# Kernel tuning notes

Measured on AMD Instinct MI355X. Metric: run time of the kernel, lower is better.

Reference implementation:

```python
import jax, jax.numpy as jnp
import numpy as np

P = 4; PSIZE = 16; EPS = 1e-8; LAM = 1e-3; MF = 2.0; ITERS = 2
BATCH = 64; A = 64; B = 8; C = 16; D = 16; E = 10


def _conv2d(x, w, b, stride, pad):
    y = jax.lax.conv_general_dilated(x, w, (stride, stride), [(pad, pad), (pad, pad)],
                                     dimension_numbers=('NCHW', 'OIHW', 'NCHW'))
    return y + b[None, :, None, None]


def _patches(x, K, stride):
    # x: (b, H, W, F) -> (b, oh, ow, K, K, F) sliding KxK windows with given stride
    b, H, W, F = x.shape
    oh = (H - K) // stride + 1
    ow = (W - K) // stride + 1
    ih = jnp.arange(oh) * stride
    iw = jnp.arange(ow) * stride
    p = x[:, ih[:, None] + jnp.arange(K)[None, :]]          # (b, oh, K, W, F)
    p = p[:, :, :, iw[:, None] + jnp.arange(K)[None, :]]    # (b, oh, K, ow, K, F)
    return p.transpose(0, 1, 3, 2, 4, 5), oh, ow


def _fuzzy_routing(v, a_in, beta_u, beta_a):
    # Fuzzy (c-means style) routing. v: (n, N, Cout, PSIZE) votes, a_in: (n, N).
    n, N, Cc, _ = v.shape
    r = jnp.full((n, N, Cc), 1.0 / Cc, dtype=v.dtype)
    aw = a_in[:, :, None]
    for t in range(ITERS):
        rm = (r ** MF) * aw                                             # fuzzified, activation-weighted
        coeff = rm / (jnp.sum(rm, axis=1, keepdims=True) + EPS)         # (n, N, C)
        mu = jnp.einsum('bnc,bncp->bcp', coeff, v)                      # (n, C, PSIZE)
        if t < ITERS - 1:
            dist = jnp.sum((v - mu[:, None]) ** 2, axis=-1) + EPS       # (n, N, C)
            inv = dist ** (-1.0 / (MF - 1.0))
            r = inv / (jnp.sum(inv, axis=2, keepdims=True) + EPS)
    sigma_sq = jnp.einsum('bnc,bncp->bcp', coeff, (v - mu[:, None]) ** 2) + EPS
    r_sum = jnp.sum((r ** MF) * aw, axis=1)                             # (n, C)
    cost = (beta_u[None, :, None] + 0.5 * jnp.log(sigma_sq)) * r_sum[:, :, None]
    a_out = jax.nn.sigmoid(LAM * (beta_a[None, :] - jnp.sum(cost, axis=2)))
    return mu, a_out


def _conv_caps(pose, a, W, beta_u, beta_a, K, stride):
    # pose: (b, H, W, Bi, PSIZE), a: (b, H, W, Bi); W: (K*K*Bi, Co, P, P)
    b, H, Wd, Bi, _ = pose.shape
    Co = W.shape[1]
    pp, oh, ow = _patches(pose.reshape(b, H, Wd, Bi * PSIZE), K, stride)
    ap, _, _ = _patches(a, K, stride)
    n = b * oh * ow
    pp = pp.reshape(n, K * K * Bi, P, P)
    ap = ap.reshape(n, K * K * Bi)
    v = jnp.einsum('nipq,icqr->nicpr', pp, W).reshape(n, K * K * Bi, Co, PSIZE)
    mu, a_out = _fuzzy_routing(v, ap, beta_u, beta_a)
    return mu.reshape(b, oh, ow, Co, PSIZE), a_out.reshape(b, oh, ow, Co)


def _class_caps(pose, a, W, beta_u, beta_a):
    # K=1, weight-shared over positions, with coordinate addition.
    b, H, Wd, Bi, _ = pose.shape
    Co = W.shape[1]
    v = jnp.einsum('bhwipq,icqr->bhwicpr', pose.reshape(b, H, Wd, Bi, P, P), W)
    v = v.reshape(b, H, Wd, Bi, Co, PSIZE)
    ch = (jnp.arange(H, dtype=v.dtype) / H)[None, :, None, None, None]
    cw = (jnp.arange(Wd, dtype=v.dtype) / Wd)[None, None, :, None, None]
    v = v.at[..., 0].add(ch)
    v = v.at[..., 1].add(cw)
    v = v.reshape(b, H * Wd * Bi, Co, PSIZE)
    return _fuzzy_routing(v, a.reshape(b, -1), beta_u, beta_a)


def setup_inputs():
    key = jax.random.key(0)
    ks = jax.random.split(key, 8)
    return {
        'x': jax.random.normal(ks[0], (BATCH, 1, 32, 32), jnp.float32),
        'conv1_w': jax.random.normal(ks[1], (A, 1, 5, 5), jnp.float32) * 0.1,
        'conv1_b': jnp.zeros((A,), jnp.float32),
        'bn_g': jnp.ones((A,), jnp.float32),
        'bn_b': jnp.zeros((A,), jnp.float32),
        'bn_mean': jnp.zeros((A,), jnp.float32),
        'bn_var': jnp.ones((A,), jnp.float32),
        'prim_pose_w': jax.random.normal(ks[2], (B * PSIZE, A, 1, 1), jnp.float32) * 0.1,
        'prim_pose_b': jnp.zeros((B * PSIZE,), jnp.float32),
        'prim_a_w': jax.random.normal(ks[3], (B, A, 1, 1), jnp.float32) * 0.1,
        'prim_a_b': jnp.zeros((B,), jnp.float32),
        'w1': jax.random.normal(ks[4], (3 * 3 * B, C, P, P), jnp.float32),
        'bu1': jnp.zeros((C,), jnp.float32),
        'ba1': jnp.zeros((C,), jnp.float32),
        'w2': jax.random.normal(ks[5], (3 * 3 * C, D, P, P), jnp.float32),
        'bu2': jnp.zeros((D,), jnp.float32),
        'ba2': jnp.zeros((D,), jnp.float32),
        'wc': jax.random.normal(ks[6], (D, E, P, P), jnp.float32),
        'buc': jnp.zeros((E,), jnp.float32),
        'bac': jnp.zeros((E,), jnp.float32),
    }


def reference(x, conv1_w, conv1_b, bn_g, bn_b, bn_mean, bn_var,
              prim_pose_w, prim_pose_b, prim_a_w, prim_a_b,
              w1, bu1, ba1, w2, bu2, ba2, wc, buc, bac):
    y = _conv2d(x, conv1_w, conv1_b, 2, 2)                               # (b, A, 16, 16)
    inv_std = jax.lax.rsqrt(bn_var + 1e-3)
    y = (y - bn_mean[None, :, None, None]) * (bn_g * inv_std)[None, :, None, None] + bn_b[None, :, None, None]
    y = jax.nn.relu(y)
    pose = _conv2d(y, prim_pose_w, prim_pose_b, 1, 0)                    # (b, B*16, 16, 16)
    a = jax.nn.sigmoid(_conv2d(y, prim_a_w, prim_a_b, 1, 0))             # (b, B, 16, 16)
    b_, _, H, Wd = a.shape
    pose = pose.transpose(0, 2, 3, 1).reshape(b_, H, Wd, B, PSIZE)
    a = a.transpose(0, 2, 3, 1)
    pose1, a1 = _conv_caps(pose, a, w1, bu1, ba1, 3, 2)
    pose2, a2 = _conv_caps(pose1, a1, w2, bu2, ba2, 3, 1)
    _, a_class = _class_caps(pose2, a2, wc, buc, bac)                    # (b, E)
    return a_class
```

## Files before the change

kernel.cpp:

```cpp
#include <hip/hip_runtime.h>
#include <math.h>

#define EPS_ 1e-8f
#define LAM_ 1e-3f

__global__ __launch_bounds__(256) void k_conv_transw(
    const float* __restrict__ x, const float* __restrict__ cw, const float* __restrict__ cb,
    const float* __restrict__ g, const float* __restrict__ bb,
    const float* __restrict__ mean, const float* __restrict__ var,
    float* __restrict__ y,
    const float* __restrict__ w1, const float* __restrict__ w2, const float* __restrict__ wc,
    const float* __restrict__ pw, const float* __restrict__ pb,
    const float* __restrict__ aw, const float* __restrict__ ab,
    float* __restrict__ w1t, float* __restrict__ w2t, float* __restrict__ wct,
    float* __restrict__ wpt)
{
    if (blockIdx.x < 4096) {
        int t = blockIdx.x * 256 + threadIdx.x;
        int ch = t & 63, w = (t >> 6) & 15, h = (t >> 10) & 15, b = t >> 14;
        const float* xb = x + b * 1024;
        const float* wc_ = cw + ch * 25;
        float acc = cb[ch];
        #pragma unroll
        for (int kh = 0; kh < 5; ++kh) {
            int ih = h * 2 - 2 + kh;
            if (ih < 0 || ih > 31) continue;
            #pragma unroll
            for (int kw = 0; kw < 5; ++kw) {
                int iw = w * 2 - 2 + kw;
                if (iw < 0 || iw > 31) continue;
                acc = fmaf(xb[ih * 32 + iw], wc_[kh * 5 + kw], acc);
            }
        }
        float v = (acc - mean[ch]) * (g[ch] * rsqrtf(var[ch] + 1e-3f)) + bb[ch];
        y[t] = fmaxf(v, 0.f);
    } else {
        int t = (blockIdx.x - 4096) * 256 + threadIdx.x;
        if (t < 3616 * 16) {
            int m = t >> 4, e = t & 15, r = e >> 2, q = e & 3;
            const float* src; float* dst;
            if (m < 1152)      { src = w1 + m * 16;          dst = w1t + m * 16; }
            else if (m < 3456) { src = w2 + (m - 1152) * 16; dst = w2t + (m - 1152) * 16; }
            else               { src = wc + (m - 3456) * 16; dst = wct + (m - 3456) * 16; }
            dst[e] = src[q * 4 + r];
        } else if (t < 3616 * 16 + 65 * 136) {
            int idx = t - 3616 * 16;
            int o = idx % 136, j = idx / 136;
            float v;
            if (j == 64)       v = (o < 128) ? pb[o] : ab[o - 128];
            else if (o < 128)  v = pw[o * 64 + j];
            else               v = aw[(o - 128) * 64 + j];
            wpt[j * 136 + o] = v;
        }
    }
}

__global__ __launch_bounds__(256) void k_prim(
    const float* __restrict__ y, const float* __restrict__ wpt,
    float* __restrict__ poseP, float* __restrict__ aP)
{
    int t = blockIdx.x * 256 + threadIdx.x;
    if (t >= 16384 * 34) return;
    int oq = t % 34;
    int pos = t / 34;
    const float* yp = y + pos * 64;
    float4 acc = *(const float4*)(wpt + 64 * 136 + oq * 4);
    #pragma unroll
    for (int j0 = 0; j0 < 64; j0 += 4) {
        float4 y4 = *(const float4*)(yp + j0);
        float4 w0 = *(const float4*)(wpt + (j0 + 0) * 136 + oq * 4);
        float4 w1 = *(const float4*)(wpt + (j0 + 1) * 136 + oq * 4);
        float4 w2 = *(const float4*)(wpt + (j0 + 2) * 136 + oq * 4);
        float4 w3 = *(const float4*)(wpt + (j0 + 3) * 136 + oq * 4);
        acc.x = fmaf(y4.x, w0.x, fmaf(y4.y, w1.x, fmaf(y4.z, w2.x, fmaf(y4.w, w3.x, acc.x))));
        acc.y = fmaf(y4.x, w0.y, fmaf(y4.y, w1.y, fmaf(y4.z, w2.y, fmaf(y4.w, w3.y, acc.y))));
        acc.z = fmaf(y4.x, w0.z, fmaf(y4.y, w1.z, fmaf(y4.z, w2.z, fmaf(y4.w, w3.z, acc.z))));
        acc.w = fmaf(y4.x, w0.w, fmaf(y4.y, w1.w, fmaf(y4.z, w2.w, fmaf(y4.w, w3.w, acc.w))));
    }
    if (oq < 32) {
        ((float4*)(poseP + pos * 128))[oq] = acc;
    } else {
        int oo = (oq - 32) * 4;
        float* ad = aP + pos * 8 + oo;
        ad[0] = 1.f / (1.f + __expf(-acc.x));
        ad[1] = 1.f / (1.f + __expf(-acc.y));
        ad[2] = 1.f / (1.f + __expf(-acc.z));
        ad[3] = 1.f / (1.f + __expf(-acc.w));
    }
}

template<int N, int C, int K, int S, int H, int W, int Bi, int OH, int OW>
__global__ __launch_bounds__(64) void k_caps_w1(
    const float* __restrict__ pose_in,
    const float* __restrict__ a_in,
    const float* __restrict__ Wt,
    const float* __restrict__ bu, const float* __restrict__ ba,
    float* __restrict__ pose_out,
    float* __restrict__ a_out)
{
    static_assert(C == 16 && N % 8 == 0, "");
    constexpr int NIT = N / 4;
    constexpr int NP  = NIT / 2;

    __shared__ __align__(16) float pp[N * 16];
    __shared__ float ap[N];

    const int lane = threadIdx.x;
    const int n_ = blockIdx.x;
    const int b = n_ / (OH * OW);
    const int rem = n_ % (OH * OW);
    const int oh = rem / OW, ow = rem % OW;

    for (int idx = lane; idx < N * 4; idx += 64) {
        int i = idx >> 2, f = idx & 3;
        int bi = i % Bi, k2 = i / Bi;
        int sw = ow * S + (k2 % K), sh = oh * S + (k2 / K);
        ((float4*)(pp + i * 16))[f] =
            ((const float4*)(pose_in + (((b * H + sh) * W + sw) * Bi + bi) * 16))[f];
    }
    for (int i = lane; i < N; i += 64) {
        int bi = i % Bi, k2 = i / Bi;
        int sw = ow * S + (k2 % K), sh = oh * S + (k2 / K);
        ap[i] = a_in[((b * H + sh) * W + sw) * Bi + bi];
    }
    __syncthreads();

    float suma = 0.f;
    for (int i = lane; i < N; i += 64) suma += ap[i];
    #pragma unroll
    for (int m = 1; m < 64; m <<= 1) suma += __shfl_xor(suma, m, 64);
    const float inv0 = __builtin_amdgcn_rcpf(suma + (float)(C * C) * EPS_);

    const int ig = (lane >> 4) & 3, cc = lane & 15;

    float mu[16];
    #pragma unroll
    for (int e2 = 0; e2 < 16; ++e2) mu[e2] = 0.f;
    for (int ii = 0; ii < NIT; ++ii) {
        int i = ig + ii * 4;
        const float4* pi4 = (const float4*)(pp + i * 16);
        const float4* wt4 = (const float4*)(Wt + (i * C + cc) * 16);
        float4 pv[4] = { pi4[0], pi4[1], pi4[2], pi4[3] };
        float4 wv[4] = { wt4[0], wt4[1], wt4[2], wt4[3] };
        float co = ap[i] * inv0;
        #pragma unroll
        for (int e2 = 0; e2 < 16; ++e2) {
            float4 p4 = pv[e2 >> 2], w4 = wv[e2 & 3];
            float v = p4.x * w4.x + p4.y * w4.y + p4.z * w4.z + p4.w * w4.w;
            mu[e2] = fmaf(co, v, mu[e2]);
        }
    }
    #pragma unroll
    for (int e2 = 0; e2 < 16; ++e2) {
        mu[e2] += __shfl_xor(mu[e2], 16, 64);
        mu[e2] += __shfl_xor(mu[e2], 32, 64);
    }

    float Sv[16], Sv2[16];
    #pragma unroll
    for (int e2 = 0; e2 < 16; ++e2) { Sv[e2] = 0.f; Sv2[e2] = 0.f; }
    float rsum = 0.f;
    for (int jj = 0; jj < NP; ++jj) {
        int i0 = ig + (2 * jj) * 4;
        int i1 = i0 + 4;
        const float4* p04 = (const float4*)(pp + i0 * 16);
        const float4* w04 = (const float4*)(Wt + (i0 * C + cc) * 16);
        const float4* p14 = (const float4*)(pp + i1 * 16);
        const float4* w14 = (const float4*)(Wt + (i1 * C + cc) * 16);
        float4 pv0[4] = { p04[0], p04[1], p04[2], p04[3] };
        float4 wv0[4] = { w04[0], w04[1], w04[2], w04[3] };
        float4 pv1[4] = { p14[0], p14[1], p14[2], p14[3] };
        float4 wv1[4] = { w14[0], w14[1], w14[2], w14[3] };
        float vv0[16], vv1[16];
        float d0 = EPS_, d1 = EPS_;
        #pragma unroll
        for (int e2 = 0; e2 < 16; ++e2) {
            float4 a4 = pv0[e2 >> 2], x4 = wv0[e2 & 3];
            float4 b4 = pv1[e2 >> 2], y4 = wv1[e2 & 3];
            float v0 = a4.x * x4.x + a4.y * x4.y + a4.z * x4.z + a4.w * x4.w;
            float v1 = b4.x * y4.x + b4.y * y4.y + b4.z * y4.z + b4.w * y4.w;
            vv0[e2] = v0; vv1[e2] = v1;
            float e0 = v0 - mu[e2];
            float e1 = v1 - mu[e2];
            d0 = fmaf(e0, e0, d0);
            d1 = fmaf(e1, e1, d1);
        }
        float inv_0 = __builtin_amdgcn_rcpf(d0);
        float inv_1 = __builtin_amdgcn_rcpf(d1);
        float s0 = inv_0, s1 = inv_1;
        #pragma unroll
        for (int m = 1; m < 16; m <<= 1) {
            s0 += __shfl_xor(s0, m, 64);
            s1 += __shfl_xor(s1, m, 64);
        }
        float r10 = inv_0 * __builtin_amdgcn_rcpf(s0 + EPS_);
        float r11 = inv_1 * __builtin_amdgcn_rcpf(s1 + EPS_);
        float rm0 = r10 * r10 * ap[i0];
        float rm1 = r11 * r11 * ap[i1];
        rsum += rm0 + rm1;
        #pragma unroll
        for (int e2 = 0; e2 < 16; ++e2) {
            float rv0 = rm0 * vv0[e2];
            float rv1 = rm1 * vv1[e2];
            Sv[e2] += rv0 + rv1;
            Sv2[e2] = fmaf(rv0, vv0[e2], fmaf(rv1, vv1[e2], Sv2[e2]));
        }
    }
    #pragma unroll
    for (int e2 = 0; e2 < 16; ++e2) {
        Sv[e2] += __shfl_xor(Sv[e2], 16, 64);
        Sv[e2] += __shfl_xor(Sv[e2], 32, 64);
        Sv2[e2] += __shfl_xor(Sv2[e2], 16, 64);
        Sv2[e2] += __shfl_xor(Sv2[e2], 32, 64);
    }
    rsum += __shfl_xor(rsum, 16, 64);
    rsum += __shfl_xor(rsum, 32, 64);

    const float id = 1.f / (rsum + EPS_);
    const float S0 = rsum * id;
    const float buc_ = bu[cc];
    float cs = 0.f;
    float4 outv[4];
    #pragma unroll
    for (int e2 = 0; e2 < 16; ++e2) {
        float sv = Sv[e2] * id;
        float sv2 = Sv2[e2] * id;
        float sigma = fmaxf(sv2 + sv * sv * (S0 - 2.f), 0.f) + EPS_;
        cs += (buc_ + 0.5f * __logf(sigma)) * rsum;
        ((float*)outv)[e2] = sv;
    }
    if (lane < 16) {
        float4* pd = (float4*)(pose_out + (n_ * C + cc) * 16);
        pd[0] = outv[0]; pd[1] = outv[1]; pd[2] = outv[2]; pd[3] = outv[3];
        a_out[n_ * C + cc] = 1.f / (1.f + __expf(-(LAM_ * (ba[cc] - cs))));
    }
}

template<int N, int C, int H, int W, int Bi, int BLK>
__global__ __launch_bounds__(BLK) void k_caps_class(
    const float* __restrict__ pose_in, const float* __restrict__ a_in,
    const float* __restrict__ Wt,
    const float* __restrict__ bu, const float* __restrict__ ba,
    float* __restrict__ a_out)
{
    constexpr int NW  = BLK / 64;
    constexpr int NIG = BLK / 16;
    constexpr int NIT = (N + NIG - 1) / NIG;

    __shared__ __align__(16) float pp[N * 16];
    __shared__ float ap[N];
    __shared__ float coeff0[N];
    __shared__ float mu0[16 * 17];
    __shared__ float red1[NW * C * 17];
    __shared__ float red2[NW * C * 17];
    __shared__ float redr[NW * C];

    const int t = threadIdx.x;
    const int lane = t & 63;
    const int w = t >> 6;
    const int b = blockIdx.x;

    for (int idx = t; idx < N * 4; idx += BLK) {
        int i = idx >> 2, f = idx & 3;
        int bi = i % Bi;
        int hw = i / Bi;
        int sw = hw % W, sh = hw / W;
        const float4* src = (const float4*)(pose_in + (((b * H + sh) * W + sw) * Bi + bi) * 16);
        ((float4*)(pp + i * 16))[f] = src[f];
    }
    for (int i = t; i < N; i += BLK) {
        int bi = i % Bi;
        int hw = i / Bi;
        int sw = hw % W, sh = hw / W;
        ap[i] = a_in[((b * H + sh) * W + sw) * Bi + bi];
    }
    __syncthreads();

    {
        float part = 0.f;
        for (int i = t; i < N; i += BLK) part += ap[i];
        #pragma unroll
        for (int m = 1; m < 64; m <<= 1) part += __shfl_xor(part, m, 64);
        if (lane == 0) red1[w] = part;
        __syncthreads();
        float s = 0.f;
        #pragma unroll
        for (int ww = 0; ww < NW; ++ww) s += red1[ww];
        float inv0 = __builtin_amdgcn_rcpf(s + (float)(C * C) * EPS_);
        for (int i = t; i < N; i += BLK) coeff0[i] = ap[i] * inv0;
        __syncthreads();
    }

    const int ig = t >> 4, cc = t & 15;

    {
        float muU[16];
        #pragma unroll
        for (int e2 = 0; e2 < 16; ++e2) muU[e2] = 0.f;
        if (cc < C) {
            for (int ii = 0; ii < NIT; ++ii) {
                int i = ig + ii * NIG;
                if (i < N) {
                    const float4* pi4 = (const float4*)(pp + i * 16);
                    const float4* wt4 = (const float4*)(Wt + ((i % Bi) * C + cc) * 16);
                    float4 pv[4] = { pi4[0], pi4[1], pi4[2], pi4[3] };
                    float4 wv[4] = { wt4[0], wt4[1], wt4[2], wt4[3] };
                    float co = coeff0[i];
                    float chv = (float)(i / (W * Bi)) * (1.f / H);
                    float cwv = (float)((i / Bi) % W) * (1.f / W);
                    #pragma unroll
                    for (int e2 = 0; e2 < 16; ++e2) {
                        float4 p4 = pv[e2 >> 2], w4 = wv[e2 & 3];
                        float v = p4.x * w4.x + p4.y * w4.y + p4.z * w4.z + p4.w * w4.w;
                        if (e2 == 0) v += chv;
                        if (e2 == 1) v += cwv;
                        muU[e2] = fmaf(co, v, muU[e2]);
                    }
                }
            }
        }
        #pragma unroll
        for (int e2 = 0; e2 < 16; ++e2) {
            float xv = muU[e2];
            xv += __shfl_xor(xv, 16, 64);
            xv += __shfl_xor(xv, 32, 64);
            if (lane < 16 && lane < C) red1[(w * C + lane) * 17 + e2] = xv;
        }
        __syncthreads();
        if (t < 256) {
            int c = t >> 4, e = t & 15;
            if (c < C) {
                float m = 0.f;
                #pragma unroll
                for (int ww = 0; ww < NW; ++ww) m += red1[(ww * C + c) * 17 + e];
                mu0[c * 17 + e] = m;
            }
        }
        __syncthreads();
    }

    {
        float m0[16];
        if (cc < C) {
            #pragma unroll
            for (int e2 = 0; e2 < 16; ++e2) m0[e2] = mu0[cc * 17 + e2];
        }
        float SvU[16], Sv2U[16];
        #pragma unroll
        for (int e2 = 0; e2 < 16; ++e2) { SvU[e2] = 0.f; Sv2U[e2] = 0.f; }
        float rsumP = 0.f;

        for (int ii = 0; ii < NIT; ++ii) {
            int i = ig + ii * NIG;
            bool act = (i < N);
            float inv = 0.f;
            float vv[16];
            if (act && cc < C) {
                const float4* pi4 = (const float4*)(pp + i * 16);
                const float4* wt4 = (const float4*)(Wt + ((i % Bi) * C + cc) * 16);
                float4 pv[4] = { pi4[0], pi4[1], pi4[2], pi4[3] };
                float4 wv[4] = { wt4[0], wt4[1], wt4[2], wt4[3] };
                float chv = (float)(i / (W * Bi)) * (1.f / H);
                float cwv = (float)((i / Bi) % W) * (1.f / W);
                float dist = EPS_;
                #pragma unroll
                for (int e2 = 0; e2 < 16; ++e2) {
                    float4 p4 = pv[e2 >> 2], w4 = wv[e2 & 3];
                    float v = p4.x * w4.x + p4.y * w4.y + p4.z * w4.z + p4.w * w4.w;
                    if (e2 == 0) v += chv;
                    if (e2 == 1) v += cwv;
                    vv[e2] = v;
                    float d = v - m0[e2];
                    dist = fmaf(d, d, dist);
                }
                inv = __builtin_amdgcn_rcpf(dist);
            }
            float s = inv;
            #pragma unroll
            for (int m = 1; m < 16; m <<= 1) s += __shfl_xor(s, m, 64);
            if (act && cc < C) {
                float r1 = inv * __builtin_amdgcn_rcpf(s + EPS_);
                float rm = r1 * r1 * ap[i];
                rsumP += rm;
                #pragma unroll
                for (int e2 = 0; e2 < 16; ++e2) {
                    SvU[e2] = fmaf(rm, vv[e2], SvU[e2]);
                    Sv2U[e2] = fmaf(rm * vv[e2], vv[e2], Sv2U[e2]);
                }
            }
        }
        #pragma unroll
        for (int e2 = 0; e2 < 16; ++e2) {
            float xv = SvU[e2];
            xv += __shfl_xor(xv, 16, 64);
            xv += __shfl_xor(xv, 32, 64);
            float yv = Sv2U[e2];
            yv += __shfl_xor(yv, 16, 64);
            yv += __shfl_xor(yv, 32, 64);
            if (lane < 16 && lane < C) {
                red1[(w * C + lane) * 17 + e2] = xv;
                red2[(w * C + lane) * 17 + e2] = yv;
            }
        }
        {
            float rv = rsumP;
            rv += __shfl_xor(rv, 16, 64);
            rv += __shfl_xor(rv, 32, 64);
            if (lane < 16 && lane < C) redr[w * C + lane] = rv;
        }
        __syncthreads();
    }

    if (t < 256) {
        int c = t >> 4, e = t & 15;
        if (c < C) {
            float SvT = 0.f, Sv2T = 0.f, R = 0.f;
            #pragma unroll
            for (int ww = 0; ww < NW; ++ww) {
                SvT  += red1[(ww * C + c) * 17 + e];
                Sv2T += red2[(ww * C + c) * 17 + e];
                R    += redr[ww * C + c];
            }
            float id = 1.f / (R + EPS_);
            float S0 = R * id;
            float Sv = SvT * id;
            float Sv2 = Sv2T * id;
            float sigma = fmaxf(Sv2 + Sv * Sv * (S0 - 2.f), 0.f) + EPS_;
            float cost = (bu[c] + 0.5f * __logf(sigma)) * R;
            float cs = cost;
            #pragma unroll
            for (int m = 1; m < 16; m <<= 1) cs += __shfl_xor(cs, m, 64);
            if (e == 0) a_out[b * C + c] = 1.f / (1.f + __expf(-(LAM_ * (ba[c] - cs))));
        }
    }
}

extern "C" void kernel_launch(void* const* d_in, const int* in_sizes, int n_in,
                              void* d_out, int out_size, void* d_ws, size_t ws_size,
                              hipStream_t stream)
{
    const float* x   = (const float*)d_in[0];
    const float* c1w = (const float*)d_in[1];
    const float* c1b = (const float*)d_in[2];
    const float* bng = (const float*)d_in[3];
    const float* bnb = (const float*)d_in[4];
    const float* bnm = (const float*)d_in[5];
    const float* bnv = (const float*)d_in[6];
    const float* ppw = (const float*)d_in[7];
    const float* ppb = (const float*)d_in[8];
    const float* paw = (const float*)d_in[9];
    const float* pab = (const float*)d_in[10];
    const float* w1  = (const float*)d_in[11];
    const float* bu1 = (const float*)d_in[12];
    const float* ba1 = (const float*)d_in[13];
    const float* w2  = (const float*)d_in[14];
    const float* bu2 = (const float*)d_in[15];
    const float* ba2 = (const float*)d_in[16];
    const float* wcp = (const float*)d_in[17];
    const float* buc = (const float*)d_in[18];
    const float* bac = (const float*)d_in[19];
    float* out = (float*)d_out;

    float* ws    = (float*)d_ws;
    float* y     = ws;
    float* poseP = y + 1048576;
    float* aP    = poseP + 2097152;
    float* pose1 = aP + 131072;
    float* a1    = pose1 + 802816;
    float* pose2 = a1 + 50176;
    float* a2    = pose2 + 409600;
    float* w1t   = a2 + 25600;
    float* w2t   = w1t + 18432;
    float* wct   = w2t + 36864;
    float* wpt   = wct + 2560;

    const int transw_blocks = (3616 * 16 + 65 * 136 + 255) / 256;
    hipLaunchKernelGGL(k_conv_transw, dim3(4096 + transw_blocks), dim3(256), 0, stream,
                       x, c1w, c1b, bng, bnb, bnm, bnv, y,
                       w1, w2, wcp, ppw, ppb, paw, pab, w1t, w2t, wct, wpt);
    hipLaunchKernelGGL(k_prim, dim3((16384 * 34 + 255) / 256), dim3(256), 0, stream,
                       y, wpt, poseP, aP);
    hipLaunchKernelGGL((k_caps_w1<72, 16, 3, 2, 16, 16, 8, 7, 7>), dim3(3136), dim3(64), 0, stream,
                       poseP, aP, w1t, bu1, ba1, pose1, a1);
    hipLaunchKernelGGL((k_caps_w1<144, 16, 3, 1, 7, 7, 16, 5, 5>), dim3(1600), dim3(64), 0, stream,
                       pose1, a1, w2t, bu2, ba2, pose2, a2);
    hipLaunchKernelGGL((k_caps_class<400, 10, 5, 5, 16, 1024>), dim3(64), dim3(1024), 0, stream,
                       pose2, a2, wct, buc, bac, out);
}
```

Before: 259.9 us.

## Rework conv-caps routing: two output caps per lane, centered moments, multi-wave blocks

The conv-caps kernel now gives each lane two output capsules and 8 input groups instead of one capsule and 4 groups, so each pose load from shared memory is reused for two vote products, and the pp rows are padded to 20 floats. The second layer runs with two wavefronts per block and combines partial sums through shared memory and barriers. Variance is now accumulated from deviations relative to the first-pass mean in both the conv and class kernels, which changes the algebra for numerical safety. The trade-off is more registers per lane, which may reduce occupancy, plus extra barrier cost in the two-wave variant.

Result: slower. 304.3 us (+17.1%).

```diff
diff --git a/kernel.cpp b/kernel.cpp
--- a/kernel.cpp
+++ b/kernel.cpp
@@ -89,8 +89,8 @@
     }
 }
 
-template<int N, int C, int K, int S, int H, int W, int Bi, int OH, int OW>
-__global__ __launch_bounds__(64) void k_caps_w1(
+template<int N, int C, int K, int S, int H, int W, int Bi, int OH, int OW, int NW>
+__global__ __launch_bounds__(NW * 64) void k_caps_c2(
     const float* __restrict__ pose_in,
     const float* __restrict__ a_in,
     const float* __restrict__ Wt,
@@ -98,27 +98,34 @@
     float* __restrict__ pose_out,
     float* __restrict__ a_out)
 {
-    static_assert(C == 16 && N % 8 == 0, "");
-    constexpr int NIT = N / 4;
-    constexpr int NP  = NIT / 2;
-
-    __shared__ __align__(16) float pp[N * 16];
+    static_assert(C == 16 && N % (NW * 8) == 0, "");
+    constexpr int BLK = NW * 64;
+    constexpr int IW  = N / NW;
+    constexpr int NIT = IW / 8;
+    constexpr int PSTR = 20;
+
+    __shared__ __align__(16) float pp[N * PSTR];
     __shared__ float ap[N];
-
-    const int lane = threadIdx.x;
+    __shared__ __align__(16) float redS[NW][8][36];
+    __shared__ __align__(16) float redQ[NW][8][36];
+    __shared__ float redR[NW][8];
+
+    const int t = threadIdx.x;
+    const int w = t >> 6, lane = t & 63;
+    const int ch = lane & 7, ig = (lane >> 3) & 7;
     const int n_ = blockIdx.x;
     const int b = n_ / (OH * OW);
     const int rem = n_ % (OH * OW);
     const int oh = rem / OW, ow = rem % OW;
 
-    for (int idx = lane; idx < N * 4; idx += 64) {
+    for (int idx = t; idx < N * 4; idx += BLK) {
         int i = idx >> 2, f = idx & 3;
         int bi = i % Bi, k2 = i / Bi;
         int sw = ow * S + (k2 % K), sh = oh * S + (k2 / K);
-        ((float4*)(pp + i * 16))[f] =
+        ((float4*)(pp + i * PSTR))[f] =
             ((const float4*)(pose_in + (((b * H + sh) * W + sw) * Bi + bi) * 16))[f];
     }
-    for (int i = lane; i < N; i += 64) {
+    for (int i = t; i < N; i += BLK) {
         int bi = i % Bi, k2 = i / Bi;
         int sw = ow * S + (k2 % K), sh = oh * S + (k2 / K);
         ap[i] = a_in[((b * H + sh) * W + sw) * Bi + bi];
@@ -131,108 +138,203 @@
     for (int m = 1; m < 64; m <<= 1) suma += __shfl_xor(suma, m, 64);
     const float inv0 = __builtin_amdgcn_rcpf(suma + (float)(C * C) * EPS_);
 
-    const int ig = (lane >> 4) & 3, cc = lane & 15;
-
-    float mu[16];
+    const int ibase = w * IW;
+    const float* WtL = Wt + 2 * ch * 16;
+
+    float mu0[16], mu1[16];
     #pragma unroll
-    for (int e2 = 0; e2 < 16; ++e2) mu[e2] = 0.f;
+    for (int e = 0; e < 16; ++e) { mu0[e] = 0.f; mu1[e] = 0.f; }
     for (int ii = 0; ii < NIT; ++ii) {
-        int i = ig + ii * 4;
-        const float4* pi4 = (const float4*)(pp + i * 16);
-        const float4* wt4 = (const float4*)(Wt + (i * C + cc) * 16);
+        int i = ibase + ig + ii * 8;
+        const float4* pi4 = (const float4*)(pp + i * PSTR);
+        const float4* wt4 = (const float4*)(WtL + i * C * 16);
         float4 pv[4] = { pi4[0], pi4[1], pi4[2], pi4[3] };
-        float4 wv[4] = { wt4[0], wt4[1], wt4[2], wt4[3] };
+        float4 w0[4] = { wt4[0], wt4[1], wt4[2], wt4[3] };
+        float4 w1[4] = { wt4[4], wt4[5], wt4[6], wt4[7] };
         float co = ap[i] * inv0;
         #pragma unroll
-        for (int e2 = 0; e2 < 16; ++e2) {
-            float4 p4 = pv[e2 >> 2], w4 = wv[e2 & 3];
-            float v = p4.x * w4.x + p4.y * w4.y + p4.z * w4.z + p4.w * w4.w;
-            mu[e2] = fmaf(co, v, mu[e2]);
+        for (int e = 0; e < 16; ++e) {
+            float4 p4 = pv[e >> 2];
+            float4 a4 = w0[e & 3], b4 = w1[e & 3];
+            float v0 = p4.x * a4.x + p4.y * a4.y + p4.z * a4.z + p4.w * a4.w;
+            float v1 = p4.x * b4.x + p4.y * b4.y + p4.z * b4.z + p4.w * b4.w;
+            mu0[e] = fmaf(co, v0, mu0[e]);
+            mu1[e] = fmaf(co, v1, mu1[e]);
         }
     }
     #pragma unroll
-    for (int e2 = 0; e2 < 16; ++e2) {
-        mu[e2] += __shfl_xor(mu[e2], 16, 64);
-        mu[e2] += __shfl_xor(mu[e2], 32, 64);
-    }
-
-    float Sv[16], Sv2[16];
+    for (int e = 0; e < 16; ++e) {
+        mu0[e] += __shfl_xor(mu0[e], 8, 64);
+        mu0[e] += __shfl_xor(mu0[e], 16, 64);
+        mu0[e] += __shfl_xor(mu0[e], 32, 64);
+        mu1[e] += __shfl_xor(mu1[e], 8, 64);
+        mu1[e] += __shfl_xor(mu1[e], 16, 64);
+        mu1[e] += __shfl_xor(mu1[e], 32, 64);
+    }
+    if constexpr (NW > 1) {
+        if (lane < 8) {
+            float4* d = (float4*)&redS[w][ch][0];
+            d[0] = *(float4*)&mu0[0]; d[1] = *(float4*)&mu0[4];
+            d[2] = *(float4*)&mu0[8]; d[3] = *(float4*)&mu0[12];
+            d[4] = *(float4*)&mu1[0]; d[5] = *(float4*)&mu1[4];
+            d[6] = *(float4*)&mu1[8]; d[7] = *(float4*)&mu1[12];
+        }
+        __syncthreads();
+        #pragma unroll
+        for (int f = 0; f < 4; ++f) {
+            float4 s0 = *(const float4*)&redS[0][ch][f * 4];
+            float4 s1 = *(const float4*)&redS[0][ch][16 + f * 4];
+            #pragma unroll
+            for (int ww = 1; ww < NW; ++ww) {
+                float4 q0 = *(const float4*)&redS[ww][ch][f * 4];
+                float4 q1 = *(const float4*)&redS[ww][ch][16 + f * 4];
+                s0.x += q0.x; s0.y += q0.y; s0.z += q0.z; s0.w += q0.w;
+                s1.x += q1.x; s1.y += q1.y; s1.z += q1.z; s1.w += q1.w;
+            }
+            *(float4*)&mu0[f * 4] = s0;
+            *(float4*)&mu1[f * 4] = s1;
+        }
+        __syncthreads();
+    }
+
+    float P2a[16], P1a[16], P2b[16], P1b[16];
     #pragma unroll
-    for (int e2 = 0; e2 < 16; ++e2) { Sv[e2] = 0.f; Sv2[e2] = 0.f; }
+    for (int e = 0; e < 16; ++e) { P2a[e] = 0.f; P1a[e] = 0.f; P2b[e] = 0.f; P1b[e] = 0.f; }
     float rsum = 0.f;
-    for (int jj = 0; jj < NP; ++jj) {
-        int i0 = ig + (2 * jj) * 4;
-        int i1 = i0 + 4;
-        const float4* p04 = (const float4*)(pp + i0 * 16);
-        const float4* w04 = (const float4*)(Wt + (i0 * C + cc) * 16);
-        const float4* p14 = (const float4*)(pp + i1 * 16);
-        const float4* w14 = (const float4*)(Wt + (i1 * C + cc) * 16);
-        float4 pv0[4] = { p04[0], p04[1], p04[2], p04[3] };
-        float4 wv0[4] = { w04[0], w04[1], w04[2], w04[3] };
-        float4 pv1[4] = { p14[0], p14[1], p14[2], p14[3] };
-        float4 wv1[4] = { w14[0], w14[1], w14[2], w14[3] };
-        float vv0[16], vv1[16];
+    for (int ii = 0; ii < NIT; ++ii) {
+        int i = ibase + ig + ii * 8;
+        const float4* pi4 = (const float4*)(pp + i * PSTR);
+        const float4* wt4 = (const float4*)(WtL + i * C * 16);
+        float4 pv[4] = { pi4[0], pi4[1], pi4[2], pi4[3] };
+        float4 w0[4] = { wt4[0], wt4[1], wt4[2], wt4[3] };
+        float4 w1[4] = { wt4[4], wt4[5], wt4[6], wt4[7] };
+        float u0[16], u1[16];
         float d0 = EPS_, d1 = EPS_;
         #pragma unroll
-        for (int e2 = 0; e2 < 16; ++e2) {
-            float4 a4 = pv0[e2 >> 2], x4 = wv0[e2 & 3];
-            float4 b4 = pv1[e2 >> 2], y4 = wv1[e2 & 3];
-            float v0 = a4.x * x4.x + a4.y * x4.y + a4.z * x4.z + a4.w * x4.w;
-            float v1 = b4.x * y4.x + b4.y * y4.y + b4.z * y4.z + b4.w * y4.w;
-            vv0[e2] = v0; vv1[e2] = v1;
-            float e0 = v0 - mu[e2];
-            float e1 = v1 - mu[e2];
+        for (int e = 0; e < 16; ++e) {
+            float4 p4 = pv[e >> 2];
+            float4 a4 = w0[e & 3], b4 = w1[e & 3];
+            float v0 = p4.x * a4.x + p4.y * a4.y + p4.z * a4.z + p4.w * a4.w;
+            float v1 = p4.x * b4.x + p4.y * b4.y + p4.z * b4.z + p4.w * b4.w;
+            float e0 = v0 - mu0[e];
+            float e1 = v1 - mu1[e];
+            u0[e] = e0; u1[e] = e1;
             d0 = fmaf(e0, e0, d0);
             d1 = fmaf(e1, e1, d1);
         }
-        float inv_0 = __builtin_amdgcn_rcpf(d0);
-        float inv_1 = __builtin_amdgcn_rcpf(d1);
-        float s0 = inv_0, s1 = inv_1;
-        #pragma unroll
-        for (int m = 1; m < 16; m <<= 1) {
-            s0 += __shfl_xor(s0, m, 64);
-            s1 += __shfl_xor(s1, m, 64);
-        }
-        float r10 = inv_0 * __builtin_amdgcn_rcpf(s0 + EPS_);
-        float r11 = inv_1 * __builtin_amdgcn_rcpf(s1 + EPS_);
-        float rm0 = r10 * r10 * ap[i0];
-        float rm1 = r11 * r11 * ap[i1];
+        float iv0 = __builtin_amdgcn_rcpf(d0);
+        float iv1 = __builtin_amdgcn_rcpf(d1);
+        float s = iv0 + iv1;
+        s += __shfl_xor(s, 1, 64);
+        s += __shfl_xor(s, 2, 64);
+        s += __shfl_xor(s, 4, 64);
+        float sinv = __builtin_amdgcn_rcpf(s + EPS_);
+        float api = ap[i];
+        float r0 = iv0 * sinv, r1 = iv1 * sinv;
+        float rm0 = r0 * r0 * api;
+        float rm1 = r1 * r1 * api;
         rsum += rm0 + rm1;
         #pragma unroll
-        for (int e2 = 0; e2 < 16; ++e2) {
-            float rv0 = rm0 * vv0[e2];
-            float rv1 = rm1 * vv1[e2];
-            Sv[e2] += rv0 + rv1;
-            Sv2[e2] = fmaf(rv0, vv0[e2], fmaf(rv1, vv1[e2], Sv2[e2]));
+        for (int e = 0; e < 16; ++e) {
+            float t0 = rm0 * u0[e];
+            float t1 = rm1 * u1[e];
+            P2a[e] += t0;
+            P2b[e] += t1;
+            P1a[e] = fmaf(t0, u0[e], P1a[e]);
+            P1b[e] = fmaf(t1, u1[e], P1b[e]);
         }
     }
     #pragma unroll
-    for (int e2 = 0; e2 < 16; ++e2) {
-        Sv[e2] += __shfl_xor(Sv[e2], 16, 64);
-        Sv[e2] += __shfl_xor(Sv[e2], 32, 64);
-        Sv2[e2] += __shfl_xor(Sv2[e2], 16, 64);
-        Sv2[e2] += __shfl_xor(Sv2[e2], 32, 64);
-    }
+    for (int e = 0; e < 16; ++e) {
+        P2a[e] += __shfl_xor(P2a[e], 8, 64);
+        P2a[e] += __shfl_xor(P2a[e], 16, 64);
+        P2a[e] += __shfl_xor(P2a[e], 32, 64);
+        P2b[e] += __shfl_xor(P2b[e], 8, 64);
+        P2b[e] += __shfl_xor(P2b[e], 16, 64);
+        P2b[e] += __shfl_xor(P2b[e], 32, 64);
+        P1a[e] += __shfl_xor(P1a[e], 8, 64);
+        P1a[e] += __shfl_xor(P1a[e], 16, 64);
+        P1a[e] += __shfl_xor(P1a[e], 32, 64);
+        P1b[e] += __shfl_xor(P1b[e], 8, 64);
+        P1b[e] += __shfl_xor(P1b[e], 16, 64);
+        P1b[e] += __shfl_xor(P1b[e], 32, 64);
+    }
+    rsum += __shfl_xor(rsum, 8, 64);
     rsum += __shfl_xor(rsum, 16, 64);
     rsum += __shfl_xor(rsum, 32, 64);
 
-    const float id = 1.f / (rsum + EPS_);
-    const float S0 = rsum * id;
-    const float buc_ = bu[cc];
-    float cs = 0.f;
-    float4 outv[4];
-    #pragma unroll
-    for (int e2 = 0; e2 < 16; ++e2) {
-        float sv = Sv[e2] * id;
-        float sv2 = Sv2[e2] * id;
-        float sigma = fmaxf(sv2 + sv * sv * (S0 - 2.f), 0.f) + EPS_;
-        cs += (buc_ + 0.5f * __logf(sigma)) * rsum;
-        ((float*)outv)[e2] = sv;
-    }
-    if (lane < 16) {
-        float4* pd = (float4*)(pose_out + (n_ * C + cc) * 16);
-        pd[0] = outv[0]; pd[1] = outv[1]; pd[2] = outv[2]; pd[3] = outv[3];
-        a_out[n_ * C + cc] = 1.f / (1.f + __expf(-(LAM_ * (ba[cc] - cs))));
+    if constexpr (NW > 1) {
+        if (lane < 8) {
+            float4* dS = (float4*)&redS[w][ch][0];
+            float4* dQ = (float4*)&redQ[w][ch][0];
+            dS[0] = *(float4*)&P2a[0]; dS[1] = *(float4*)&P2a[4];
+            dS[2] = *(float4*)&P2a[8]; dS[3] = *(float4*)&P2a[12];
+            dS[4] = *(float4*)&P2b[0]; dS[5] = *(float4*)&P2b[4];
+            dS[6] = *(float4*)&P2b[8]; dS[7] = *(float4*)&P2b[12];
+            dQ[0] = *(float4*)&P1a[0]; dQ[1] = *(float4*)&P1a[4];
+            dQ[2] = *(float4*)&P1a[8]; dQ[3] = *(float4*)&P1a[12];
+            dQ[4] = *(float4*)&P1b[0]; dQ[5] = *(float4*)&P1b[4];
+            dQ[6] = *(float4*)&P1b[8]; dQ[7] = *(float4*)&P1b[12];
+            redR[w][ch] = rsum;
+        }
+        __syncthreads();
+    }
+
+    if (w == 0 && lane < 8) {
+        if constexpr (NW > 1) {
+            #pragma unroll
+            for (int f = 0; f < 4; ++f) {
+                float4 s0 = *(const float4*)&redS[0][ch][f * 4];
+                float4 s1 = *(const float4*)&redS[0][ch][16 + f * 4];
+                float4 q0 = *(const float4*)&redQ[0][ch][f * 4];
+                float4 q1 = *(const float4*)&redQ[0][ch][16 + f * 4];
+                #pragma unroll
+                for (int ww = 1; ww < NW; ++ww) {
+                    float4 a0 = *(const float4*)&redS[ww][ch][f * 4];
+                    float4 a1 = *(const float4*)&redS[ww][ch][16 + f * 4];
+                    float4 b0 = *(const float4*)&redQ[ww][ch][f * 4];
+                    float4 b1 = *(const float4*)&redQ[ww][ch][16 + f * 4];
+                    s0.x += a0.x; s0.y += a0.y; s0.z += a0.z; s0.w += a0.w;
+                    s1.x += a1.x; s1.y += a1.y; s1.z += a1.z; s1.w += a1.w;
+                    q0.x += b0.x; q0.y += b0.y; q0.z += b0.z; q0.w += b0.w;
+                    q1.x += b1.x; q1.y += b1.y; q1.z += b1.z; q1.w += b1.w;
+                }
+                *(float4*)&P2a[f * 4] = s0;
+                *(float4*)&P2b[f * 4] = s1;
+                *(float4*)&P1a[f * 4] = q0;
+                *(float4*)&P1b[f * 4] = q1;
+            }
+            rsum = 0.f;
+            #pragma unroll
+            for (int ww = 0; ww < NW; ++ww) rsum += redR[ww][ch];
+        }
+        const int c0 = 2 * ch;
+        const float id = 1.f / (rsum + EPS_);
+        const float S0 = rsum * id;
+        float cs0 = 0.f, cs1 = 0.f;
+        const float bu0 = bu[c0], bu1 = bu[c0 + 1];
+        float4 out0[4], out1[4];
+        #pragma unroll
+        for (int e = 0; e < 16; ++e) {
+            float p2 = P2a[e] * id;
+            float dm = mu0[e] * (S0 - 1.f) + p2;
+            float sg = P1a[e] * id - 2.f * dm * p2 + dm * dm * S0;
+            sg = fmaxf(sg, 0.f) + EPS_;
+            cs0 += (bu0 + 0.5f * __logf(sg)) * rsum;
+            ((float*)out0)[e] = mu0[e] + dm;
+
+            float q2 = P2b[e] * id;
+            float dn = mu1[e] * (S0 - 1.f) + q2;
+            float sh2 = P1b[e] * id - 2.f * dn * q2 + dn * dn * S0;
+            sh2 = fmaxf(sh2, 0.f) + EPS_;
+            cs1 += (bu1 + 0.5f * __logf(sh2)) * rsum;
+            ((float*)out1)[e] = mu1[e] + dn;
+        }
+        float4* pd = (float4*)(pose_out + (n_ * C + c0) * 16);
+        pd[0] = out0[0]; pd[1] = out0[1]; pd[2] = out0[2]; pd[3] = out0[3];
+        pd[4] = out1[0]; pd[5] = out1[1]; pd[6] = out1[2]; pd[7] = out1[3];
+        a_out[n_ * C + c0]     = 1.f / (1.f + __expf(-(LAM_ * (ba[c0] - cs0))));
+        a_out[n_ * C + c0 + 1] = 1.f / (1.f + __expf(-(LAM_ * (ba[c0 + 1] - cs1))));
     }
 }
 
@@ -345,16 +447,16 @@
             #pragma unroll
             for (int e2 = 0; e2 < 16; ++e2) m0[e2] = mu0[cc * 17 + e2];
         }
-        float SvU[16], Sv2U[16];
-        #pragma unroll
-        for (int e2 = 0; e2 < 16; ++e2) { SvU[e2] = 0.f; Sv2U[e2] = 0.f; }
+        float P2[16], P1[16];
+        #pragma unroll
+        for (int e2 = 0; e2 < 16; ++e2) { P2[e2] = 0.f; P1[e2] = 0.f; }
         float rsumP = 0.f;
 
         for (int ii = 0; ii < NIT; ++ii) {
             int i = ig + ii * NIG;
             bool act = (i < N);
             float inv = 0.f;
-            float vv[16];
+            float uu[16];
             if (act && cc < C) {
                 const float4* pi4 = (const float4*)(pp + i * 16);
                 const float4* wt4 = (const float4*)(Wt + ((i % Bi) * C + cc) * 16);
@@ -369,8 +471,8 @@
                     float v = p4.x * w4.x + p4.y * w4.y + p4.z * w4.z + p4.w * w4.w;
                     if (e2 == 0) v += chv;
                     if (e2 == 1) v += cwv;
-                    vv[e2] = v;
                     float d = v - m0[e2];
+                    uu[e2] = d;
                     dist = fmaf(d, d, dist);
                 }
                 inv = __builtin_amdgcn_rcpf(dist);
@@ -384,17 +486,18 @@
                 rsumP += rm;
                 #pragma unroll
                 for (int e2 = 0; e2 < 16; ++e2) {
-                    SvU[e2] = fmaf(rm, vv[e2], SvU[e2]);
-                    Sv2U[e2] = fmaf(rm * vv[e2], vv[e2], Sv2U[e2]);
+                    float tu = rm * uu[e2];
+                    P2[e2] += tu;
+                    P1[e2] = fmaf(tu, uu[e2], P1[e2]);
                 }
             }
         }
         #pragma unroll
         for (int e2 = 0; e2 < 16; ++e2) {
-            float xv = SvU[e2];
+            float xv = P2[e2];
             xv += __shfl_xor(xv, 16, 64);
             xv += __shfl_xor(xv, 32, 64);
-            float yv = Sv2U[e2];
+            float yv = P1[e2];
             yv += __shfl_xor(yv, 16, 64);
             yv += __shfl_xor(yv, 32, 64);
             if (lane < 16 && lane < C) {
@@ -414,18 +517,20 @@
     if (t < 256) {
         int c = t >> 4, e = t & 15;
         if (c < C) {
-            float SvT = 0.f, Sv2T = 0.f, R = 0.f;
+            float P2T = 0.f, P1T = 0.f, R = 0.f;
             #pragma unroll
             for (int ww = 0; ww < NW; ++ww) {
-                SvT  += red1[(ww * C + c) * 17 + e];
-                Sv2T += red2[(ww * C + c) * 17 + e];
-                R    += redr[ww * C + c];
+                P2T += red1[(ww * C + c) * 17 + e];
+                P1T += red2[(ww * C + c) * 17 + e];
+                R   += redr[ww * C + c];
             }
             float id = 1.f / (R + EPS_);
             float S0 = R * id;
-            float Sv = SvT * id;
-            float Sv2 = Sv2T * id;
-            float sigma = fmaxf(Sv2 + Sv * Sv * (S0 - 2.f), 0.f) + EPS_;
+            float m0v = mu0[c * 17 + e];
+            float p2 = P2T * id;
+            float dm = m0v * (S0 - 1.f) + p2;
+            float sigma = P1T * id - 2.f * dm * p2 + dm * dm * S0;
+            sigma = fmaxf(sigma, 0.f) + EPS_;
             float cost = (bu[c] + 0.5f * __logf(sigma)) * R;
             float cs = cost;
             #pragma unroll
@@ -480,9 +585,9 @@
                        w1, w2, wcp, ppw, ppb, paw, pab, w1t, w2t, wct, wpt);
     hipLaunchKernelGGL(k_prim, dim3((16384 * 34 + 255) / 256), dim3(256), 0, stream,
                        y, wpt, poseP, aP);
-    hipLaunchKernelGGL((k_caps_w1<72, 16, 3, 2, 16, 16, 8, 7, 7>), dim3(3136), dim3(64), 0, stream,
+    hipLaunchKernelGGL((k_caps_c2<72, 16, 3, 2, 16, 16, 8, 7, 7, 1>), dim3(3136), dim3(64), 0, stream,
                        poseP, aP, w1t, bu1, ba1, pose1, a1);
-    hipLaunchKernelGGL((k_caps_w1<144, 16, 3, 1, 7, 7, 16, 5, 5>), dim3(1600), dim3(64), 0, stream,
+    hipLaunchKernelGGL((k_caps_c2<144, 16, 3, 1, 7, 7, 16, 5, 5, 2>), dim3(1600), dim3(128), 0, stream,
                        pose1, a1, w2t, bu2, ba2, pose2, a2);
     hipLaunchKernelGGL((k_caps_class<400, 10, 5, 5, 16, 1024>), dim3(64), dim3(1024), 0, stream,
                        pose2, a2, wct, buc, bac, out);
```
